# Kernel tuning notes

Measured on AMD Instinct MI355X. Metric: run time of the kernel, lower is better.

## Reference

```python
import jax, jax.numpy as jnp
import numpy as np

N = 100000   # nodes
E = 1200000  # edges
IN = 128     # in_channels
H = 64       # hidden_channels


def setup_inputs() -> dict:
    key = jax.random.key(0)
    ks = jax.random.split(key, 8)
    x = jax.random.normal(ks[0], (N, IN), jnp.float32)
    edge_index = jax.random.randint(ks[1], (2, E), 0, N, dtype=jnp.int32)
    W_pre = jax.random.normal(ks[2], (IN, H), jnp.float32) * (1.0 / np.sqrt(IN))
    b_pre = jnp.zeros((H,), jnp.float32)
    W1 = jax.random.normal(ks[3], (H, H), jnp.float32) * (1.0 / np.sqrt(H))
    b1 = jnp.zeros((H,), jnp.float32)
    W2 = jax.random.normal(ks[4], (H, H), jnp.float32) * (1.0 / np.sqrt(H))
    b2 = jnp.zeros((H,), jnp.float32)
    return {"x": x, "edge_index": edge_index, "W_pre": W_pre, "b_pre": b_pre,
            "W1": W1, "b1": b1, "W2": W2, "b2": b2}


def _gcn_conv(x, src, dst, W, b, n):
    # PyG GCNConv: x' = D^{-1/2} (A + I) D^{-1/2} (x @ W) + b
    x = x @ W                                   # [N, H]
    deg = jax.ops.segment_sum(jnp.ones_like(dst, jnp.float32), dst, num_segments=n)
    dinv = jnp.where(deg > 0, jax.lax.rsqrt(jnp.maximum(deg, 1e-12)), 0.0)
    norm = dinv[src] * dinv[dst]                # [E+N]
    msg = x[src] * norm[:, None]                # gather + scale, [E+N, H]
    out = jax.ops.segment_sum(msg, dst, num_segments=n)  # scatter-add, [N, H]
    return out + b


def reference(x, edge_index, W_pre, b_pre, W1, b1, W2, b2):
    n = x.shape[0]
    loop = jnp.arange(n, dtype=edge_index.dtype)
    # add self-loops once (same structure both layers)
    src = jnp.concatenate([edge_index[0], loop])
    dst = jnp.concatenate([edge_index[1], loop])
    x = x @ W_pre + b_pre
    ori_x = x
    x = jax.nn.relu(_gcn_conv(x, src, dst, W1, b1, n))
    x = jax.nn.relu(_gcn_conv(x, src, dst, W2, b2, n))
    return (x, ori_x)
```

## Files before the change

### kernel.cpp

```cpp
#include <hip/hip_runtime.h>

#define H 64
#define SLOTS 64

typedef __attribute__((ext_vector_type(8))) short short8;
typedef __attribute__((ext_vector_type(4))) float floatx4;
typedef __attribute__((ext_vector_type(8))) unsigned short ushort8v;

static __device__ __forceinline__ unsigned short f2bf(float f) {
  union { float f; unsigned u; } x{f};
  unsigned r = x.u + 0x7fffu + ((x.u >> 16) & 1u);
  return (unsigned short)(r >> 16);
}
static __device__ __forceinline__ float bf2f(unsigned short u) {
  union { unsigned u; float f; } x{(unsigned)u << 16};
  return x.f;
}


__global__ __launch_bounds__(256) void hdr_init_kernel(int* __restrict__ csr64, int N) {
  int i = blockIdx.x * 256 + threadIdx.x;
  if (i < N) csr64[(size_t)i * SLOTS] = 0;
}

__global__ __launch_bounds__(256) void edge_scatter_kernel(const int* __restrict__ src,
                                                           const int* __restrict__ dst,
                                                           int* __restrict__ csr64, int E) {
  int e = blockIdx.x * 256 + threadIdx.x;
  if (e >= E) return;
  int s = src[e];
  int d = dst[e];
  int r = atomicAdd(&csr64[(size_t)d * SLOTS], 1);
  if (r < SLOTS - 1)
    csr64[(size_t)d * SLOTS + 1 + r] = s;
}


__global__ __launch_bounds__(256) void prep_kernel(const float* __restrict__ Wpre,
                                                   const float* __restrict__ W1,
                                                   const float* __restrict__ W2,
                                                   unsigned short* __restrict__ frag,
                                                   const int* __restrict__ csr64,
                                                   float* __restrict__ dinv, int N) {
  int i = blockIdx.x * 256 + threadIdx.x;
  if (i < 16384) {
    const float* W;
    int K, base;
    if (i < 8192) {
      W = Wpre; K = 128; base = 0;
    } else if (i < 12288) {
      W = W1; K = 64; base = 8192;
    } else {
      W = W2; K = 64; base = 12288;
    }
    int s = i - base;
    int j = s & 7;
    int t = s >> 3;
    int l = t & 63;
    int t2 = t >> 6;
    int KB = K / 32;
    int kb = t2 % KB;
    int w = t2 / KB;
    int k = kb * 32 + ((l >> 4) & 3) * 8 + j;
    int n = w * 16 + (l & 15);
    frag[i] = f2bf(W[k * H + n]);
  }
  int j = i - 16384;
  if (j >= 0 && j < N)
    dinv[j] = rsqrtf((float)csr64[(size_t)j * SLOTS] + 1.0f);
}


__global__ __launch_bounds__(256) void fused_gemm_kernel(
    const float* __restrict__ X, const unsigned short* __restrict__ Wfrag,
    const float* __restrict__ bpre, const float* __restrict__ dinv,
    float* __restrict__ ori, unsigned short* __restrict__ g, int N) {
  __shared__ __align__(16) unsigned short As[4 * 64 * 8];
  __shared__ __align__(16) unsigned short os[16 * 72];
  __shared__ float dinv_s[16];
  const int tid = threadIdx.x;
  const int w = tid >> 6;
  const int lane = tid & 63;
  const int row0 = blockIdx.x * 16;

  {
    int kb = tid >> 6;
    int l = tid & 63;
    int m = l & 15;
    int k0 = kb * 32 + (l >> 4) * 8;
    int r = row0 + m;
    ushort8v v = {0, 0, 0, 0, 0, 0, 0, 0};
    if (r < N) {
      const float* xp = &X[(size_t)r * 128 + k0];
      float4 a = *(const float4*)xp;
      float4 b = *(const float4*)(xp + 4);
      v = ushort8v{f2bf(a.x), f2bf(a.y), f2bf(a.z), f2bf(a.w),
                   f2bf(b.x), f2bf(b.y), f2bf(b.z), f2bf(b.w)};
    }
    *(ushort8v*)&As[(kb * 64 + l) * 8] = v;
  }
  if (tid < 16) dinv_s[tid] = (row0 + tid < N) ? dinv[row0 + tid] : 1.f;

  short8 bfragP[4], bfrag1[2];
  {
    const unsigned short* wf = &Wfrag[((size_t)(w * 4) * 64 + lane) * 8];
#pragma unroll
    for (int kb = 0; kb < 4; ++kb) bfragP[kb] = *(const short8*)&wf[kb * 512];
    const unsigned short* wf1 = &Wfrag[8192 + ((size_t)(w * 2) * 64 + lane) * 8];
#pragma unroll
    for (int kb = 0; kb < 2; ++kb) bfrag1[kb] = *(const short8*)&wf1[kb * 512];
  }
  __syncthreads();

  floatx4 accP = {0.f, 0.f, 0.f, 0.f};
#pragma unroll
  for (int kb = 0; kb < 4; ++kb) {
    short8 a = *(const short8*)&As[(kb * 64 + lane) * 8];
    accP = __builtin_amdgcn_mfma_f32_16x16x32_bf16(a, bfragP[kb], accP, 0, 0, 0);
  }

  const int c = w * 16 + (lane & 15);
  const int q = lane >> 4;
  {
    float bv = bpre[c];
#pragma unroll
    for (int r = 0; r < 4; ++r) {
      int m = q * 4 + r;
      int row = row0 + m;
      float v = accP[r] + bv;
      if (row < N) ori[(size_t)row * H + c] = v;
      os[m * 72 + c] = f2bf(v);
    }
  }
  __syncthreads();

  floatx4 acc2 = {0.f, 0.f, 0.f, 0.f};
#pragma unroll
  for (int kb = 0; kb < 2; ++kb) {
    short8 a = *(const short8*)&os[(lane & 15) * 72 + kb * 32 + (lane >> 4) * 8];
    acc2 = __builtin_amdgcn_mfma_f32_16x16x32_bf16(a, bfrag1[kb], acc2, 0, 0, 0);
  }
#pragma unroll
  for (int r = 0; r < 4; ++r) {
    int row = row0 + q * 4 + r;
    if (row < N) g[(size_t)row * H + c] = f2bf(acc2[r] * dinv_s[q * 4 + r]);
  }
}


static __device__ __forceinline__ float gather_rows(const unsigned short* __restrict__ g,
                                                    int hv, int deg, int lane, int zrow) {
  float acc = 0.f;
#pragma unroll
  for (int b = 0; b < 4; ++b) {
    if (b * 16 < deg) {
      float x[16];
#pragma unroll
      for (int u = 0; u < 16; ++u) {
        int slot = b * 16 + 1 + u;
        int sidx = (slot < SLOTS) ? __builtin_amdgcn_readlane(hv, slot) : zrow;
        sidx = (slot <= deg) ? sidx : zrow;
        x[u] = bf2f(g[(size_t)sidx * H + lane]);
      }
#pragma unroll
      for (int u = 0; u < 16; ++u) acc += x[u];
    }
  }
  return acc;
}


__global__ __launch_bounds__(1024) void gather_fused_kernel(
    const unsigned short* __restrict__ g, const int* __restrict__ csr64,
    const float* __restrict__ bias, const unsigned short* __restrict__ w2frag,
    unsigned short* __restrict__ out, int N) {
  __shared__ __align__(16) unsigned short os[16 * 72];
  __shared__ float dinv_s[16];
  const int tid = threadIdx.x;
  const int w = tid >> 6;
  const int lane = tid & 63;
  const int node0 = blockIdx.x * 16;
  const int node = node0 + w;

  float x1 = 0.f;
  if (node < N) {
    int hv = csr64[(size_t)node * SLOTS + lane];
    float self = bf2f(g[(size_t)node * H + lane]);
    float bl = bias[lane];
    int degt = __builtin_amdgcn_readlane(hv, 0);
    float dn = rsqrtf((float)degt + 1.0f);
    int deg = min(degt, SLOTS - 1);
    float acc = self + gather_rows(g, csr64 ? hv : 0, deg, lane, N);
    x1 = fmaxf(fmaf(dn, acc, bl), 0.f);
    if (lane == 0) dinv_s[w] = dn;
  }
  os[w * 72 + lane] = f2bf(x1);
  __syncthreads();

  if (w < 4) {
    short8 bfrag[2];
#pragma unroll
    for (int kb = 0; kb < 2; ++kb)
      bfrag[kb] = *(const short8*)&w2frag[((size_t)(w * 2 + kb) * 64 + lane) * 8];
    floatx4 acc2 = {0.f, 0.f, 0.f, 0.f};
#pragma unroll
    for (int kb = 0; kb < 2; ++kb) {
      short8 a = *(const short8*)&os[(lane & 15) * 72 + kb * 32 + (lane >> 4) * 8];
      acc2 = __builtin_amdgcn_mfma_f32_16x16x32_bf16(a, bfrag[kb], acc2, 0, 0, 0);
    }
    const int c = w * 16 + (lane & 15);
    const int q = lane >> 4;
#pragma unroll
    for (int r = 0; r < 4; ++r) {
      int row = node0 + q * 4 + r;
      if (row < N) out[(size_t)row * H + c] = f2bf(acc2[r] * dinv_s[q * 4 + r]);
    }
  }
}


__global__ __launch_bounds__(256) void gather_kernel(const unsigned short* __restrict__ g,
                                                     const int* __restrict__ csr64,
                                                     const float* __restrict__ bias,
                                                     float* __restrict__ out, int N) {
  int node = (blockIdx.x * 256 + threadIdx.x) >> 6;
  int c = threadIdx.x & 63;
  if (node >= N) return;

  int hv = csr64[(size_t)node * SLOTS + c];
  float self = bf2f(g[(size_t)node * H + c]);
  float bl = bias[c];
  int degt = __builtin_amdgcn_readlane(hv, 0);
  float dn = rsqrtf((float)degt + 1.0f);
  int deg = min(degt, SLOTS - 1);
  float acc = self + gather_rows(g, hv, deg, c, N);
  out[(size_t)node * H + c] = fmaxf(fmaf(dn, acc, bl), 0.f);
}


extern "C" void kernel_launch(void* const* d_in, const int* in_sizes, int n_in,
                              void* d_out, int out_size, void* d_ws, size_t ws_size,
                              hipStream_t stream) {
  const float* x = (const float*)d_in[0];
  const int* ei = (const int*)d_in[1];
  const float* W_pre = (const float*)d_in[2];
  const float* b_pre = (const float*)d_in[3];
  const float* W1 = (const float*)d_in[4];
  const float* b1 = (const float*)d_in[5];
  const float* W2 = (const float*)d_in[6];
  const float* b2 = (const float*)d_in[7];

  const int IN = 128;
  const int N = in_sizes[0] / IN;
  const int E = in_sizes[1] / 2;
  const int* src = ei;
  const int* dst = ei + E;

  float* out = (float*)d_out;
  float* ori = out + (size_t)N * H;

  char* p = (char*)d_ws;
  auto take = [&](size_t bytes) {
    char* q = p;
    p += (bytes + 255) & ~(size_t)255;
    return q;
  };
  int* csr64 = (int*)take((size_t)N * SLOTS * 4);
  float* dinv = (float*)take((size_t)N * 4);
  unsigned short* g1 = (unsigned short*)take((size_t)(N + 1) * H * 2);
  unsigned short* g2 = (unsigned short*)take((size_t)(N + 1) * H * 2);
  unsigned short* wfrag = (unsigned short*)take(16384 * 2);

  hipMemsetAsync(g1 + (size_t)N * H, 0, H * 2, stream);
  hipMemsetAsync(g2 + (size_t)N * H, 0, H * 2, stream);

  hdr_init_kernel<<<(N + 255) / 256, 256, 0, stream>>>(csr64, N);
  edge_scatter_kernel<<<(E + 255) / 256, 256, 0, stream>>>(src, dst, csr64, E);
  prep_kernel<<<(16384 + N + 255) / 256, 256, 0, stream>>>(W_pre, W1, W2, wfrag,
                                                           csr64, dinv, N);

  int gb = (N + 15) / 16;
  int nb = (N + 3) / 4;

  fused_gemm_kernel<<<gb, 256, 0, stream>>>(x, wfrag, b_pre, dinv, ori, g1, N);
  gather_fused_kernel<<<gb, 1024, 0, stream>>>(g1, csr64, b1, wfrag + 12288, g2, N);
  gather_kernel<<<nb, 256, 0, stream>>>(g2, csr64, b2, out, N);
}
```

Before: 255.2 us.

## Build adjacency slabs via two-pass bucketed scatter instead of global atomics

Replaces the per-edge global atomic scatter into the 64-slot adjacency slabs with a two-pass scheme. The first pass bins edges into 128-node buckets using shared-memory counters and one global cursor atomic per bucket per chunk. The second pass builds each bucket's slabs with shared-memory atomics and computes dinv in the same kernel. This aims to cut contended random global atomics and scattered writes, at the cost of an extra packed edge buffer, a fixed per-bucket capacity that could overflow for skewed degree distributions, and src packed into 25 bits.

```diff
diff --git a/kernel.cpp b/kernel.cpp
--- a/kernel.cpp
+++ b/kernel.cpp
@@ -2,6 +2,11 @@
 
 #define H 64
 #define SLOTS 64
+#define NPB 128
+#define BSHIFT 7
+#define CAP 2048
+#define CHUNK 4096
+#define CPAD 16
 
 typedef __attribute__((ext_vector_type(8))) short short8;
 typedef __attribute__((ext_vector_type(4))) float floatx4;
@@ -18,56 +23,107 @@
 }
 
 
-__global__ __launch_bounds__(256) void hdr_init_kernel(int* __restrict__ csr64, int N) {
+__global__ __launch_bounds__(512) void bucket_scatter_kernel(const int* __restrict__ src,
+                                                             const int* __restrict__ dst,
+                                                             int* __restrict__ gcursor,
+                                                             unsigned int* __restrict__ bpk,
+                                                             int E, int NB) {
+  __shared__ int cnt[1024];
+  __shared__ int base[1024];
+  int t = threadIdx.x;
+  for (int i = t; i < NB; i += 512) cnt[i] = 0;
+  __syncthreads();
+  int cbase = blockIdx.x * CHUNK;
+  int s[CHUNK / 512], d[CHUNK / 512];
+#pragma unroll
+  for (int j = 0; j < CHUNK / 512; ++j) {
+    int e = cbase + j * 512 + t;
+    s[j] = (e < E) ? src[e] : -1;
+    d[j] = (e < E) ? dst[e] : -1;
+    if (d[j] >= 0) atomicAdd(&cnt[d[j] >> BSHIFT], 1);
+  }
+  __syncthreads();
+  for (int i = t; i < NB; i += 512)
+    base[i] = cnt[i] ? (i * CAP + atomicAdd(&gcursor[i * CPAD], cnt[i])) : 0;
+  __syncthreads();
+  for (int i = t; i < NB; i += 512) cnt[i] = 0;
+  __syncthreads();
+#pragma unroll
+  for (int j = 0; j < CHUNK / 512; ++j) {
+    if (d[j] >= 0) {
+      int b = d[j] >> BSHIFT;
+      int r = atomicAdd(&cnt[b], 1);
+      int slot = base[b] + r;
+      if (slot < (b + 1) * CAP)
+        bpk[slot] = ((unsigned)s[j] << BSHIFT) | (unsigned)(d[j] & (NPB - 1));
+    }
+  }
+}
+
+
+__global__ __launch_bounds__(256) void slab_build_kernel(const unsigned int* __restrict__ bpk,
+                                                         const int* __restrict__ gcursor,
+                                                         int* __restrict__ csr64,
+                                                         float* __restrict__ dinv, int N) {
+  __shared__ int cnt[NPB];
+  __shared__ int woff[NPB];
+  const int b = blockIdx.x;
+  const int t = threadIdx.x;
+  if (t < NPB) cnt[t] = 0;
+  __syncthreads();
+  const int beg = b * CAP;
+  const int end = beg + min(gcursor[b * CPAD], CAP);
+  for (int e = beg + t; e < end; e += 256)
+    atomicAdd(&cnt[bpk[e] & (NPB - 1)], 1);
+  __syncthreads();
+
+  if (t < NPB) {
+    int node = b * NPB + t;
+    if (node < N) {
+      csr64[(size_t)node * SLOTS] = cnt[t];
+      dinv[node] = rsqrtf((float)cnt[t] + 1.0f);
+    }
+    woff[t] = 0;
+  }
+  __syncthreads();
+
+  for (int e = beg + t; e < end; e += 256) {
+    unsigned pk = bpk[e];
+    int nl = (int)(pk & (NPB - 1));
+    int r = atomicAdd(&woff[nl], 1);
+    if (r < SLOTS - 1)
+      csr64[((size_t)(b * NPB + nl)) * SLOTS + 1 + r] = (int)(pk >> BSHIFT);
+  }
+}
+
+
+__global__ __launch_bounds__(256) void wprep_kernel(const float* __restrict__ Wpre,
+                                                    const float* __restrict__ W1,
+                                                    const float* __restrict__ W2,
+                                                    unsigned short* __restrict__ frag) {
   int i = blockIdx.x * 256 + threadIdx.x;
-  if (i < N) csr64[(size_t)i * SLOTS] = 0;
-}
-
-__global__ __launch_bounds__(256) void edge_scatter_kernel(const int* __restrict__ src,
-                                                           const int* __restrict__ dst,
-                                                           int* __restrict__ csr64, int E) {
-  int e = blockIdx.x * 256 + threadIdx.x;
-  if (e >= E) return;
-  int s = src[e];
-  int d = dst[e];
-  int r = atomicAdd(&csr64[(size_t)d * SLOTS], 1);
-  if (r < SLOTS - 1)
-    csr64[(size_t)d * SLOTS + 1 + r] = s;
-}
-
-
-__global__ __launch_bounds__(256) void prep_kernel(const float* __restrict__ Wpre,
-                                                   const float* __restrict__ W1,
-                                                   const float* __restrict__ W2,
-                                                   unsigned short* __restrict__ frag,
-                                                   const int* __restrict__ csr64,
-                                                   float* __restrict__ dinv, int N) {
-  int i = blockIdx.x * 256 + threadIdx.x;
-  if (i < 16384) {
-    const float* W;
-    int K, base;
-    if (i < 8192) {
-      W = Wpre; K = 128; base = 0;
-    } else if (i < 12288) {
-      W = W1; K = 64; base = 8192;
-    } else {
-      W = W2; K = 64; base = 12288;
-    }
-    int s = i - base;
-    int j = s & 7;
-    int t = s >> 3;
-    int l = t & 63;
-    int t2 = t >> 6;
-    int KB = K / 32;
-    int kb = t2 % KB;
-    int w = t2 / KB;
-    int k = kb * 32 + ((l >> 4) & 3) * 8 + j;
-    int n = w * 16 + (l & 15);
-    frag[i] = f2bf(W[k * H + n]);
-  }
-  int j = i - 16384;
-  if (j >= 0 && j < N)
-    dinv[j] = rsqrtf((float)csr64[(size_t)j * SLOTS] + 1.0f);
+  const float* W;
+  int K, base;
+  if (i < 8192) {
+    W = Wpre; K = 128; base = 0;
+  } else if (i < 12288) {
+    W = W1; K = 64; base = 8192;
+  } else if (i < 16384) {
+    W = W2; K = 64; base = 12288;
+  } else {
+    return;
+  }
+  int s = i - base;
+  int j = s & 7;
+  int t = s >> 3;
+  int l = t & 63;
+  int t2 = t >> 6;
+  int KB = K / 32;
+  int kb = t2 % KB;
+  int w = t2 / KB;
+  int k = kb * 32 + ((l >> 4) & 3) * 8 + j;
+  int n = w * 16 + (l & 15);
+  frag[i] = f2bf(W[k * H + n]);
 }
 
 
@@ -190,7 +246,7 @@
     int degt = __builtin_amdgcn_readlane(hv, 0);
     float dn = rsqrtf((float)degt + 1.0f);
     int deg = min(degt, SLOTS - 1);
-    float acc = self + gather_rows(g, csr64 ? hv : 0, deg, lane, N);
+    float acc = self + gather_rows(g, hv, deg, lane, N);
     x1 = fmaxf(fmaf(dn, acc, bl), 0.f);
     if (lane == 0) dinv_s[w] = dn;
   }
@@ -255,6 +311,7 @@
   const int E = in_sizes[1] / 2;
   const int* src = ei;
   const int* dst = ei + E;
+  const int NB = (N + NPB - 1) / NPB;
 
   float* out = (float*)d_out;
   float* ori = out + (size_t)N * H;
@@ -265,19 +322,22 @@
     p += (bytes + 255) & ~(size_t)255;
     return q;
   };
+  int* gcursor = (int*)take(1024 * CPAD * 4);
+  float* dinv = (float*)take((size_t)N * 4);
+  unsigned int* bpk = (unsigned int*)take((size_t)NB * CAP * 4);
   int* csr64 = (int*)take((size_t)N * SLOTS * 4);
-  float* dinv = (float*)take((size_t)N * 4);
   unsigned short* g1 = (unsigned short*)take((size_t)(N + 1) * H * 2);
   unsigned short* g2 = (unsigned short*)take((size_t)(N + 1) * H * 2);
   unsigned short* wfrag = (unsigned short*)take(16384 * 2);
 
+  hipMemsetAsync(gcursor, 0, (size_t)NB * CPAD * 4, stream);
   hipMemsetAsync(g1 + (size_t)N * H, 0, H * 2, stream);
   hipMemsetAsync(g2 + (size_t)N * H, 0, H * 2, stream);
 
-  hdr_init_kernel<<<(N + 255) / 256, 256, 0, stream>>>(csr64, N);
-  edge_scatter_kernel<<<(E + 255) / 256, 256, 0, stream>>>(src, dst, csr64, E);
-  prep_kernel<<<(16384 + N + 255) / 256, 256, 0, stream>>>(W_pre, W1, W2, wfrag,
-                                                           csr64, dinv, N);
+  int eb = (E + CHUNK - 1) / CHUNK;
+  bucket_scatter_kernel<<<eb, 512, 0, stream>>>(src, dst, gcursor, bpk, E, NB);
+  slab_build_kernel<<<NB, 256, 0, stream>>>(bpk, gcursor, csr64, dinv, N);
+  wprep_kernel<<<64, 256, 0, stream>>>(W_pre, W1, W2, wfrag);
 
   int gb = (N + 15) / 16;
   int nb = (N + 3) / 4;
```

After: 234.9 us. 8.0% less time.
